# Performance work log

Measured on AMD Instinct MI355X. Metric: run time of the kernel, lower is better.

## Reference

```python
import jax, jax.numpy as jnp
import numpy as np

N = 100000       # nodes
E = 3200000      # edges (before self-loops)
F_IN = 256       # input feature dim
HID = 32         # GCNConv output dim
CLASSES = 10


def setup_inputs() -> dict:
    key = jax.random.key(0)
    k1, k2, k3, k4 = jax.random.split(key, 4)
    feature = jax.random.normal(k1, (N, F_IN), dtype=jnp.float32)
    edge_index = jax.random.randint(k2, (2, E), 0, N, dtype=jnp.int64)
    W1 = jax.random.normal(k3, (F_IN, HID), dtype=jnp.float32) * (1.0 / np.sqrt(F_IN))
    b1 = jnp.zeros((HID,), dtype=jnp.float32)
    W2 = jax.random.normal(k4, (HID, CLASSES), dtype=jnp.float32) * (1.0 / np.sqrt(HID))
    b2 = jnp.zeros((CLASSES,), dtype=jnp.float32)
    return {"feature": feature, "edge_index": edge_index,
            "W1": W1, "b1": b1, "W2": W2, "b2": b2}


def reference(feature, edge_index, W1, b1, W2, b2):
    # --- GCNConv(features, 32): PyG semantics ---
    # add self-loops
    loops = jnp.arange(N, dtype=edge_index.dtype)
    row = jnp.concatenate([edge_index[0], loops])   # source nodes
    col = jnp.concatenate([edge_index[1], loops])   # target nodes
    # linear transform before propagation
    h = feature @ W1                                # [N, HID]
    # symmetric deg^{-1/2} normalization (degree counted at targets)
    deg = jax.ops.segment_sum(jnp.ones_like(col, dtype=h.dtype), col,
                              num_segments=N)       # [N], >=1 due to self-loops
    dinv = jax.lax.rsqrt(deg)
    norm = dinv[row] * dinv[col]                    # [E+N]
    # gather-scale-scatter aggregation
    msg = h[row] * norm[:, None]                    # [E+N, HID]
    agg = jax.ops.segment_sum(msg, col, num_segments=N) + b1  # [N, HID]
    # --- relu, (dropout: identity in eval), final linear, log_softmax ---
    act = jax.nn.relu(agg)
    logits = act @ W2 + b2                          # [N, CLASSES]
    return jax.nn.log_softmax(logits, axis=1)
```

## Files before the change

kernel.cpp:

```cpp
#include <hip/hip_runtime.h>
#include <hip/hip_fp16.h>

constexpr int N_NODES = 100000;
constexpr int E_EDGES = 3200000;
constexpr int F_IN    = 256;
constexpr int HID     = 32;
constexpr int NCLS    = 10;

constexpr int BUCK_SHIFT = 7;
constexpr int NPB        = 128;
constexpr int NBUCK      = (N_NODES + NPB - 1) / NPB;
constexpr int EPB        = 8192;
constexpr int NBLK1      = (E_EDGES + EPB - 1) / EPB;
constexpr int CAP        = 6144;

constexpr size_t OFF_FLAG = 0;
constexpr size_t OFF_GCUR = 4u << 10;
constexpr size_t OFF_W1F  = 32u << 10;
constexpr size_t OFF_CNT  = 1u << 20;
constexpr size_t OFF_OFF  = 3u << 20;
constexpr size_t OFF_DINV = 4u << 20;
constexpr size_t OFF_CSR  = 5u << 20;
constexpr size_t OFF_BIN  = 25u << 20;
constexpr size_t OFF_HS   = 25u << 20;

typedef __attribute__((ext_vector_type(8))) short bf16x8;
typedef __attribute__((ext_vector_type(4))) float f32x4;

__device__ __forceinline__ unsigned pack_bf16x2(float a, float b) {
    unsigned ua = __float_as_uint(a), ub = __float_as_uint(b);
    ua = (ua + 0x7FFFu + ((ua >> 16) & 1u)) >> 16;
    ub = (ub + 0x7FFFu + ((ub >> 16) & 1u)) >> 16;
    return ua | (ub << 16);
}
__device__ __forceinline__ __half2 u2h(unsigned u) {
    union { unsigned u; __half2 h; } v; v.u = u; return v.h;
}

__device__ __forceinline__ int load_idx(const void* ei, long long i, int is64) {
    if (is64) return (int)((const long long*)ei)[i];
    return ((const int*)ei)[i];
}

__global__ __launch_bounds__(1024) void k_initw(const int* __restrict__ ei32,
                                                int* __restrict__ flag,
                                                int* __restrict__ gcur,
                                                const float* __restrict__ W1,
                                                unsigned* __restrict__ w1f) {
    __shared__ int nz;
    int tid = threadIdx.x;
    if (tid == 0) nz = 0;
    __syncthreads();
    if (ei32[2 * tid + 1] != 0) atomicOr(&nz, 1);
    __syncthreads();
    if (tid == 0) flag[0] = (nz == 0) ? 1 : 0;
    if (tid < NBUCK) gcur[tid] = tid * CAP;

    #pragma unroll
    for (int q = 0; q < 4; q++) {
        int i = tid + q * 1024;
        int p    = i & 3;
        int lane = (i >> 2) & 63;
        int f    = i >> 8;
        int ks = f >> 1, t = f & 1;
        int kg = lane >> 4, col = lane & 15;
        int k0 = ks * 32 + kg * 8 + p * 2;
        float w0 = W1[k0 * HID + t * 16 + col];
        float w1 = W1[(k0 + 1) * HID + t * 16 + col];
        w1f[i] = pack_bf16x2(w0, w1);
    }
}

__global__ __launch_bounds__(1024) void k_scat(const void* __restrict__ ei,
                                               const int* __restrict__ flag,
                                               int* __restrict__ gcur,
                                               unsigned* __restrict__ binned) {
    __shared__ int h[NBUCK];
    __shared__ int cur[NBUCK];
    int tid = threadIdx.x, blk = blockIdx.x;
    for (int i = tid; i < NBUCK; i += 1024) h[i] = 0;
    __syncthreads();

    int is64 = flag[0];
    int base = blk * EPB;
    int nedge = min(EPB, E_EDGES - base);

    unsigned val[8];
    int      bk[8];
    #pragma unroll
    for (int j = 0; j < 8; j++) {
        int k = tid + j * 1024;
        if (k < nedge) {
            int i = base + k;
            int r = load_idx(ei, i, is64);
            int c = load_idx(ei, (long long)E_EDGES + i, is64);
            bk[j]  = c >> BUCK_SHIFT;
            val[j] = ((unsigned)r << BUCK_SHIFT) | ((unsigned)c & (NPB - 1));
            atomicAdd(&h[bk[j]], 1);
        } else {
            bk[j] = -1;
        }
    }
    __syncthreads();

    for (int j = tid; j < NBUCK; j += 1024) {
        int c = h[j];
        cur[j] = (c > 0) ? atomicAdd(&gcur[j], c) : 0;
    }
    __syncthreads();

    #pragma unroll
    for (int j = 0; j < 8; j++) {
        if (bk[j] >= 0) {
            int d = atomicAdd(&cur[bk[j]], 1);
            binned[d] = val[j];
        }
    }
}

__global__ __launch_bounds__(1024) void k_p2(const unsigned* __restrict__ binned,
                                             const int* __restrict__ gcur,
                                             int* __restrict__ cnt,
                                             int* __restrict__ off,
                                             float* __restrict__ dinv,
                                             int* __restrict__ csr) {
    __shared__ unsigned sval[CAP];
    __shared__ int lcnt[NPB], sc[NPB], lcur[NPB];
    int b = blockIdx.x, tid = threadIdx.x;
    int s = b * CAP;
    int m = gcur[b] - s;
    if (tid < NPB) lcnt[tid] = 0;
    __syncthreads();
    for (int i = tid; i < m; i += 1024) {
        unsigned p = binned[s + i];
        sval[i] = p;
        atomicAdd(&lcnt[p & (NPB - 1)], 1);
    }
    __syncthreads();
    if (tid < NPB) sc[tid] = lcnt[tid];
    __syncthreads();
    for (int d = 1; d < NPB; d <<= 1) {
        int t = 0;
        if (tid < NPB && tid >= d) t = sc[tid - d];
        __syncthreads();
        if (tid < NPB) sc[tid] += t;
        __syncthreads();
    }
    if (tid < NPB) {
        int o = s + sc[tid] - lcnt[tid];
        lcur[tid] = o;
        int node = b * NPB + tid;
        if (node < N_NODES) {
            off[node]  = o;
            cnt[node]  = lcnt[tid];
            dinv[node] = rsqrtf((float)lcnt[tid] + 1.0f);
        }
    }
    __syncthreads();
    for (int i = tid; i < m; i += 1024) {
        unsigned p = sval[i];
        int pos = atomicAdd(&lcur[p & (NPB - 1)], 1);
        csr[pos] = (int)(p >> BUCK_SHIFT);
    }
}

__global__ __launch_bounds__(256) void k_h(const float* __restrict__ feat,
                                           const unsigned* __restrict__ w1f,
                                           const float* __restrict__ dinv,
                                           unsigned short* __restrict__ hs16s) {
    int tid  = threadIdx.x;
    int lane = tid & 63;
    long wid = (long)blockIdx.x * 4 + (tid >> 6);
    int n0 = (int)(wid * 16);
    if (n0 >= N_NODES) return;

    bf16x8 bfrag[16];
    const bf16x8* wv = (const bf16x8*)w1f;
    #pragma unroll
    for (int f = 0; f < 16; f++) bfrag[f] = wv[f * 64 + lane];

    int arow = lane & 15;
    int kg   = lane >> 4;
    const float4* fr = (const float4*)(feat + (size_t)(n0 + arow) * F_IN);

    f32x4 acc0 = {0.f, 0.f, 0.f, 0.f};
    f32x4 acc1 = {0.f, 0.f, 0.f, 0.f};

    #pragma unroll
    for (int ks = 0; ks < 8; ks++) {
        float4 fa = fr[ks * 8 + kg * 2 + 0];
        float4 fb = fr[ks * 8 + kg * 2 + 1];
        unsigned au[4];
        au[0] = pack_bf16x2(fa.x, fa.y);
        au[1] = pack_bf16x2(fa.z, fa.w);
        au[2] = pack_bf16x2(fb.x, fb.y);
        au[3] = pack_bf16x2(fb.z, fb.w);
        bf16x8 af = *(bf16x8*)au;
        acc0 = __builtin_amdgcn_mfma_f32_16x16x32_bf16(af, bfrag[ks * 2 + 0], acc0, 0, 0, 0);
        acc1 = __builtin_amdgcn_mfma_f32_16x16x32_bf16(af, bfrag[ks * 2 + 1], acc1, 0, 0, 0);
    }

    int rb = kg * 4;
    #pragma unroll
    for (int r = 0; r < 4; r++) {
        int node = n0 + rb + r;
        float di = dinv[node];
        hs16s[(size_t)node * HID + arow]      = __half_as_ushort(__float2half(acc0[r] * di));
        hs16s[(size_t)node * HID + 16 + arow] = __half_as_ushort(__float2half(acc1[r] * di));
    }
}

__global__ __launch_bounds__(256) void k_aggout(const int* __restrict__ off,
                                                const int* __restrict__ cnt,
                                                const int* __restrict__ csr,
                                                const unsigned* __restrict__ hs16,
                                                const float* __restrict__ dinv,
                                                const float* __restrict__ b1,
                                                const float* __restrict__ W2,
                                                const float* __restrict__ b2,
                                                float* __restrict__ out) {
    __shared__ float W2s[HID * NCLS];
    __shared__ float b2s[NCLS];
    int tid = threadIdx.x;
    for (int i = tid; i < HID * NCLS; i += 256) W2s[i] = W2[i];
    if (tid < NCLS) b2s[tid] = b2[tid];
    __syncthreads();

    int l2   = tid & 3;
    int g    = tid >> 2;
    int node = blockIdx.x * 64 + g;
    if (node >= N_NODES) return;

    int o = off[node];
    int n = cnt[node];

    const uint4* hsv = (const uint4*)hs16;
    uint4 ps = hsv[(size_t)node * 4 + l2];
    __half2 s0 = u2h(ps.x), s1 = u2h(ps.y), s2 = u2h(ps.z), s3 = u2h(ps.w);

    #define ADDQ(Q) \
        s0 = __hadd2(s0, u2h(Q.x)); s1 = __hadd2(s1, u2h(Q.y)); \
        s2 = __hadd2(s2, u2h(Q.z)); s3 = __hadd2(s3, u2h(Q.w));

    int i = 0;
    for (; i + 8 <= n; i += 8) {
        int r0 = csr[o + i + 0];
        int r1 = csr[o + i + 1];
        int r2 = csr[o + i + 2];
        int r3 = csr[o + i + 3];
        int r4 = csr[o + i + 4];
        int r5 = csr[o + i + 5];
        int r6 = csr[o + i + 6];
        int r7 = csr[o + i + 7];
        uint4 q0 = hsv[(size_t)r0 * 4 + l2];
        uint4 q1 = hsv[(size_t)r1 * 4 + l2];
        uint4 q2 = hsv[(size_t)r2 * 4 + l2];
        uint4 q3 = hsv[(size_t)r3 * 4 + l2];
        uint4 q4 = hsv[(size_t)r4 * 4 + l2];
        uint4 q5 = hsv[(size_t)r5 * 4 + l2];
        uint4 q6 = hsv[(size_t)r6 * 4 + l2];
        uint4 q7 = hsv[(size_t)r7 * 4 + l2];
        ADDQ(q0) ADDQ(q1) ADDQ(q2) ADDQ(q3)
        ADDQ(q4) ADDQ(q5) ADDQ(q6) ADDQ(q7)
    }
    for (; i < n; i++) {
        uint4 q = hsv[(size_t)csr[o + i] * 4 + l2];
        ADDQ(q)
    }
    #undef ADDQ

    float2 f0 = __half22float2(s0);
    float2 f1 = __half22float2(s1);
    float2 f2 = __half22float2(s2);
    float2 f3 = __half22float2(s3);

    float di = dinv[node];
    float4 b1lo = *(const float4*)(b1 + 8 * l2);
    float4 b1hi = *(const float4*)(b1 + 8 * l2 + 4);
    float act[8];
    act[0] = fmaxf(b1lo.x + f0.x * di, 0.f);
    act[1] = fmaxf(b1lo.y + f0.y * di, 0.f);
    act[2] = fmaxf(b1lo.z + f1.x * di, 0.f);
    act[3] = fmaxf(b1lo.w + f1.y * di, 0.f);
    act[4] = fmaxf(b1hi.x + f2.x * di, 0.f);
    act[5] = fmaxf(b1hi.y + f2.y * di, 0.f);
    act[6] = fmaxf(b1hi.z + f3.x * di, 0.f);
    act[7] = fmaxf(b1hi.w + f3.y * di, 0.f);

    float p[NCLS];
    #pragma unroll
    for (int c = 0; c < NCLS; c++) {
        float s = 0.f;
        #pragma unroll
        for (int k = 0; k < 8; k++) s = fmaf(act[k], W2s[(8 * l2 + k) * NCLS + c], s);
        p[c] = s;
    }

    #pragma unroll
    for (int d = 1; d < 4; d <<= 1) {
        #pragma unroll
        for (int c = 0; c < NCLS; c++) p[c] += __shfl_xor(p[c], d, 4);
    }

    #pragma unroll
    for (int c = 0; c < NCLS; c++) p[c] += b2s[c];
    float m = p[0];
    #pragma unroll
    for (int c = 1; c < NCLS; c++) m = fmaxf(m, p[c]);
    float se = 0.f;
    #pragma unroll
    for (int c = 0; c < NCLS; c++) se += expf(p[c] - m);
    float lse = m + logf(se);

    #pragma unroll
    for (int q = 0; q < 3; q++) {
        int c = l2 + 4 * q;
        if (c < NCLS) {
            float v = p[0];
            #pragma unroll
            for (int cc = 1; cc < NCLS; cc++) v = (c == cc) ? p[cc] : v;
            out[(size_t)node * NCLS + c] = v - lse;
        }
    }
}

extern "C" void kernel_launch(void* const* d_in, const int* in_sizes, int n_in,
                              void* d_out, int out_size, void* d_ws, size_t ws_size,
                              hipStream_t stream) {
    const float* feat = (const float*)d_in[0];
    const void*  ei   = d_in[1];
    const float* W1   = (const float*)d_in[2];
    const float* b1   = (const float*)d_in[3];
    const float* W2   = (const float*)d_in[4];
    const float* b2   = (const float*)d_in[5];
    float* out = (float*)d_out;

    char* ws = (char*)d_ws;
    int*      flag   = (int*)(ws + OFF_FLAG);
    int*      gcur   = (int*)(ws + OFF_GCUR);
    unsigned* w1f    = (unsigned*)(ws + OFF_W1F);
    int*      cnt    = (int*)(ws + OFF_CNT);
    int*      off    = (int*)(ws + OFF_OFF);
    float*    dinv   = (float*)(ws + OFF_DINV);
    int*      csr    = (int*)(ws + OFF_CSR);
    unsigned* binned = (unsigned*)(ws + OFF_BIN);
    unsigned* hs16   = (unsigned*)(ws + OFF_HS);

    k_initw<<<1, 1024, 0, stream>>>((const int*)ei, flag, gcur, W1, w1f);
    k_scat<<<NBLK1, 1024, 0, stream>>>(ei, flag, gcur, binned);
    k_p2<<<NBUCK, 1024, 0, stream>>>(binned, gcur, cnt, off, dinv, csr);

    k_h<<<(N_NODES / 16 + 3) / 4, 256, 0, stream>>>(feat, w1f, dinv,
                                                    (unsigned short*)hs16);
    k_aggout<<<(N_NODES + 63) / 64, 256, 0, stream>>>(off, cnt, csr, hs16, dinv,
                                                      b1, W2, b2, out);
}
```

Before: 119.8 us.

## Split hidden features into two halves and aggregate in two cache-friendly passes

The fp16 hidden feature table is stored as two separate 16-column halves. Aggregation runs as two kernels, each gathering only one half, so each pass works on a smaller gather table that may fit better in L2 and cut the miss traffic of random neighbor gathers. The first pass writes partial logits to a workspace buffer, and the second adds them before log_softmax. The cost is reading the CSR index array and offsets twice, plus an extra partial-logit write and read. The feature transform kernel now handles 32 nodes per wave so it can write both halves.

```diff
diff --git a/kernel.cpp b/kernel.cpp
--- a/kernel.cpp
+++ b/kernel.cpp
@@ -22,7 +22,9 @@
 constexpr size_t OFF_DINV = 4u << 20;
 constexpr size_t OFF_CSR  = 5u << 20;
 constexpr size_t OFF_BIN  = 25u << 20;
-constexpr size_t OFF_HS   = 25u << 20;
+constexpr size_t OFF_HSA  = 25u << 20;
+constexpr size_t OFF_HSB  = 29u << 20;
+constexpr size_t OFF_PART = 33u << 20;
 
 typedef __attribute__((ext_vector_type(8))) short bf16x8;
 typedef __attribute__((ext_vector_type(4))) float f32x4;
@@ -167,11 +169,12 @@
 __global__ __launch_bounds__(256) void k_h(const float* __restrict__ feat,
                                            const unsigned* __restrict__ w1f,
                                            const float* __restrict__ dinv,
-                                           unsigned short* __restrict__ hs16s) {
+                                           unsigned short* __restrict__ hsA,
+                                           unsigned short* __restrict__ hsB) {
     int tid  = threadIdx.x;
     int lane = tid & 63;
     long wid = (long)blockIdx.x * 4 + (tid >> 6);
-    int n0 = (int)(wid * 16);
+    int n0 = (int)(wid * 32);
     if (n0 >= N_NODES) return;
 
     bf16x8 bfrag[16];
@@ -181,44 +184,142 @@
 
     int arow = lane & 15;
     int kg   = lane >> 4;
-    const float4* fr = (const float4*)(feat + (size_t)(n0 + arow) * F_IN);
-
-    f32x4 acc0 = {0.f, 0.f, 0.f, 0.f};
-    f32x4 acc1 = {0.f, 0.f, 0.f, 0.f};
+    const float4* frA = (const float4*)(feat + (size_t)(n0 + arow) * F_IN);
+    const float4* frB = (const float4*)(feat + (size_t)(n0 + 16 + arow) * F_IN);
+
+    f32x4 acc0a = {0.f, 0.f, 0.f, 0.f};
+    f32x4 acc1a = {0.f, 0.f, 0.f, 0.f};
+    f32x4 acc0b = {0.f, 0.f, 0.f, 0.f};
+    f32x4 acc1b = {0.f, 0.f, 0.f, 0.f};
 
     #pragma unroll
     for (int ks = 0; ks < 8; ks++) {
-        float4 fa = fr[ks * 8 + kg * 2 + 0];
-        float4 fb = fr[ks * 8 + kg * 2 + 1];
-        unsigned au[4];
-        au[0] = pack_bf16x2(fa.x, fa.y);
-        au[1] = pack_bf16x2(fa.z, fa.w);
-        au[2] = pack_bf16x2(fb.x, fb.y);
-        au[3] = pack_bf16x2(fb.z, fb.w);
-        bf16x8 af = *(bf16x8*)au;
-        acc0 = __builtin_amdgcn_mfma_f32_16x16x32_bf16(af, bfrag[ks * 2 + 0], acc0, 0, 0, 0);
-        acc1 = __builtin_amdgcn_mfma_f32_16x16x32_bf16(af, bfrag[ks * 2 + 1], acc1, 0, 0, 0);
+        float4 faA = frA[ks * 8 + kg * 2 + 0];
+        float4 fbA = frA[ks * 8 + kg * 2 + 1];
+        float4 faB = frB[ks * 8 + kg * 2 + 0];
+        float4 fbB = frB[ks * 8 + kg * 2 + 1];
+        unsigned auA[4], auB[4];
+        auA[0] = pack_bf16x2(faA.x, faA.y);
+        auA[1] = pack_bf16x2(faA.z, faA.w);
+        auA[2] = pack_bf16x2(fbA.x, fbA.y);
+        auA[3] = pack_bf16x2(fbA.z, fbA.w);
+        auB[0] = pack_bf16x2(faB.x, faB.y);
+        auB[1] = pack_bf16x2(faB.z, faB.w);
+        auB[2] = pack_bf16x2(fbB.x, fbB.y);
+        auB[3] = pack_bf16x2(fbB.z, fbB.w);
+        bf16x8 afA = *(bf16x8*)auA;
+        bf16x8 afB = *(bf16x8*)auB;
+        acc0a = __builtin_amdgcn_mfma_f32_16x16x32_bf16(afA, bfrag[ks * 2 + 0], acc0a, 0, 0, 0);
+        acc1a = __builtin_amdgcn_mfma_f32_16x16x32_bf16(afA, bfrag[ks * 2 + 1], acc1a, 0, 0, 0);
+        acc0b = __builtin_amdgcn_mfma_f32_16x16x32_bf16(afB, bfrag[ks * 2 + 0], acc0b, 0, 0, 0);
+        acc1b = __builtin_amdgcn_mfma_f32_16x16x32_bf16(afB, bfrag[ks * 2 + 1], acc1b, 0, 0, 0);
     }
 
     int rb = kg * 4;
     #pragma unroll
     for (int r = 0; r < 4; r++) {
-        int node = n0 + rb + r;
-        float di = dinv[node];
-        hs16s[(size_t)node * HID + arow]      = __half_as_ushort(__float2half(acc0[r] * di));
-        hs16s[(size_t)node * HID + 16 + arow] = __half_as_ushort(__float2half(acc1[r] * di));
-    }
-}
-
-__global__ __launch_bounds__(256) void k_aggout(const int* __restrict__ off,
-                                                const int* __restrict__ cnt,
-                                                const int* __restrict__ csr,
-                                                const unsigned* __restrict__ hs16,
-                                                const float* __restrict__ dinv,
-                                                const float* __restrict__ b1,
-                                                const float* __restrict__ W2,
-                                                const float* __restrict__ b2,
-                                                float* __restrict__ out) {
+        int nodeA = n0 + rb + r;
+        float diA = dinv[nodeA];
+        hsA[(size_t)nodeA * 16 + arow] = __half_as_ushort(__float2half(acc0a[r] * diA));
+        hsB[(size_t)nodeA * 16 + arow] = __half_as_ushort(__float2half(acc1a[r] * diA));
+        int nodeB = n0 + 16 + rb + r;
+        float diB = dinv[nodeB];
+        hsA[(size_t)nodeB * 16 + arow] = __half_as_ushort(__float2half(acc0b[r] * diB));
+        hsB[(size_t)nodeB * 16 + arow] = __half_as_ushort(__float2half(acc1b[r] * diB));
+    }
+}
+
+__global__ __launch_bounds__(256) void k_aggA(const int* __restrict__ off,
+                                              const int* __restrict__ cnt,
+                                              const int* __restrict__ csr,
+                                              const unsigned short* __restrict__ hsA,
+                                              const float* __restrict__ dinv,
+                                              const float* __restrict__ b1,
+                                              const float* __restrict__ W2,
+                                              float* __restrict__ partial) {
+    __shared__ float W2s[HID * NCLS];
+    int tid = threadIdx.x;
+    for (int i = tid; i < HID * NCLS; i += 256) W2s[i] = W2[i];
+    __syncthreads();
+
+    int l    = tid & 1;
+    int g    = tid >> 1;
+    int node = blockIdx.x * 128 + g;
+    if (node >= N_NODES) return;
+
+    int o = off[node];
+    int n = cnt[node];
+
+    const uint4* hv = (const uint4*)hsA;
+    uint4 ps = hv[(size_t)node * 2 + l];
+    __half2 s0 = u2h(ps.x), s1 = u2h(ps.y), s2 = u2h(ps.z), s3 = u2h(ps.w);
+
+    #define ADDQ(Q) \
+        s0 = __hadd2(s0, u2h(Q.x)); s1 = __hadd2(s1, u2h(Q.y)); \
+        s2 = __hadd2(s2, u2h(Q.z)); s3 = __hadd2(s3, u2h(Q.w));
+    int i = 0;
+    for (; i + 8 <= n; i += 8) {
+        int r0 = csr[o + i + 0], r1 = csr[o + i + 1], r2 = csr[o + i + 2], r3 = csr[o + i + 3];
+        int r4 = csr[o + i + 4], r5 = csr[o + i + 5], r6 = csr[o + i + 6], r7 = csr[o + i + 7];
+        uint4 q0 = hv[(size_t)r0 * 2 + l], q1 = hv[(size_t)r1 * 2 + l];
+        uint4 q2 = hv[(size_t)r2 * 2 + l], q3 = hv[(size_t)r3 * 2 + l];
+        uint4 q4 = hv[(size_t)r4 * 2 + l], q5 = hv[(size_t)r5 * 2 + l];
+        uint4 q6 = hv[(size_t)r6 * 2 + l], q7 = hv[(size_t)r7 * 2 + l];
+        ADDQ(q0) ADDQ(q1) ADDQ(q2) ADDQ(q3) ADDQ(q4) ADDQ(q5) ADDQ(q6) ADDQ(q7)
+    }
+    for (; i < n; i++) {
+        uint4 q = hv[(size_t)csr[o + i] * 2 + l];
+        ADDQ(q)
+    }
+    #undef ADDQ
+
+    float2 f0 = __half22float2(s0), f1 = __half22float2(s1);
+    float2 f2 = __half22float2(s2), f3 = __half22float2(s3);
+    float di = dinv[node];
+    int kb = 8 * l;
+    float4 blo = *(const float4*)(b1 + kb);
+    float4 bhi = *(const float4*)(b1 + kb + 4);
+    float act[8];
+    act[0] = fmaxf(blo.x + f0.x * di, 0.f);
+    act[1] = fmaxf(blo.y + f0.y * di, 0.f);
+    act[2] = fmaxf(blo.z + f1.x * di, 0.f);
+    act[3] = fmaxf(blo.w + f1.y * di, 0.f);
+    act[4] = fmaxf(bhi.x + f2.x * di, 0.f);
+    act[5] = fmaxf(bhi.y + f2.y * di, 0.f);
+    act[6] = fmaxf(bhi.z + f3.x * di, 0.f);
+    act[7] = fmaxf(bhi.w + f3.y * di, 0.f);
+
+    float p[NCLS];
+    #pragma unroll
+    for (int c = 0; c < NCLS; c++) {
+        float s = 0.f;
+        #pragma unroll
+        for (int k = 0; k < 8; k++) s = fmaf(act[k], W2s[(kb + k) * NCLS + c], s);
+        p[c] = s;
+    }
+    #pragma unroll
+    for (int c = 0; c < NCLS; c++) p[c] += __shfl_xor(p[c], 1, 2);
+
+    #pragma unroll
+    for (int j = 0; j < 5; j++) {
+        int c = 5 * l + j;
+        float v = p[0];
+        #pragma unroll
+        for (int cc = 1; cc < NCLS; cc++) v = (c == cc) ? p[cc] : v;
+        partial[(size_t)node * NCLS + c] = v;
+    }
+}
+
+__global__ __launch_bounds__(256) void k_aggB(const int* __restrict__ off,
+                                              const int* __restrict__ cnt,
+                                              const int* __restrict__ csr,
+                                              const unsigned short* __restrict__ hsB,
+                                              const float* __restrict__ dinv,
+                                              const float* __restrict__ b1,
+                                              const float* __restrict__ W2,
+                                              const float* __restrict__ b2,
+                                              const float* __restrict__ partial,
+                                              float* __restrict__ out) {
     __shared__ float W2s[HID * NCLS];
     __shared__ float b2s[NCLS];
     int tid = threadIdx.x;
@@ -226,84 +327,68 @@
     if (tid < NCLS) b2s[tid] = b2[tid];
     __syncthreads();
 
-    int l2   = tid & 3;
-    int g    = tid >> 2;
-    int node = blockIdx.x * 64 + g;
+    int l    = tid & 1;
+    int g    = tid >> 1;
+    int node = blockIdx.x * 128 + g;
     if (node >= N_NODES) return;
 
     int o = off[node];
     int n = cnt[node];
 
-    const uint4* hsv = (const uint4*)hs16;
-    uint4 ps = hsv[(size_t)node * 4 + l2];
+    const uint4* hv = (const uint4*)hsB;
+    uint4 ps = hv[(size_t)node * 2 + l];
     __half2 s0 = u2h(ps.x), s1 = u2h(ps.y), s2 = u2h(ps.z), s3 = u2h(ps.w);
 
     #define ADDQ(Q) \
         s0 = __hadd2(s0, u2h(Q.x)); s1 = __hadd2(s1, u2h(Q.y)); \
         s2 = __hadd2(s2, u2h(Q.z)); s3 = __hadd2(s3, u2h(Q.w));
-
     int i = 0;
     for (; i + 8 <= n; i += 8) {
-        int r0 = csr[o + i + 0];
-        int r1 = csr[o + i + 1];
-        int r2 = csr[o + i + 2];
-        int r3 = csr[o + i + 3];
-        int r4 = csr[o + i + 4];
-        int r5 = csr[o + i + 5];
-        int r6 = csr[o + i + 6];
-        int r7 = csr[o + i + 7];
-        uint4 q0 = hsv[(size_t)r0 * 4 + l2];
-        uint4 q1 = hsv[(size_t)r1 * 4 + l2];
-        uint4 q2 = hsv[(size_t)r2 * 4 + l2];
-        uint4 q3 = hsv[(size_t)r3 * 4 + l2];
-        uint4 q4 = hsv[(size_t)r4 * 4 + l2];
-        uint4 q5 = hsv[(size_t)r5 * 4 + l2];
-        uint4 q6 = hsv[(size_t)r6 * 4 + l2];
-        uint4 q7 = hsv[(size_t)r7 * 4 + l2];
-        ADDQ(q0) ADDQ(q1) ADDQ(q2) ADDQ(q3)
-        ADDQ(q4) ADDQ(q5) ADDQ(q6) ADDQ(q7)
+        int r0 = csr[o + i + 0], r1 = csr[o + i + 1], r2 = csr[o + i + 2], r3 = csr[o + i + 3];
+        int r4 = csr[o + i + 4], r5 = csr[o + i + 5], r6 = csr[o + i + 6], r7 = csr[o + i + 7];
+        uint4 q0 = hv[(size_t)r0 * 2 + l], q1 = hv[(size_t)r1 * 2 + l];
+        uint4 q2 = hv[(size_t)r2 * 2 + l], q3 = hv[(size_t)r3 * 2 + l];
+        uint4 q4 = hv[(size_t)r4 * 2 + l], q5 = hv[(size_t)r5 * 2 + l];
+        uint4 q6 = hv[(size_t)r6 * 2 + l], q7 = hv[(size_t)r7 * 2 + l];
+        ADDQ(q0) ADDQ(q1) ADDQ(q2) ADDQ(q3) ADDQ(q4) ADDQ(q5) ADDQ(q6) ADDQ(q7)
     }
     for (; i < n; i++) {
-        uint4 q = hsv[(size_t)csr[o + i] * 4 + l2];
+        uint4 q = hv[(size_t)csr[o + i] * 2 + l];
         ADDQ(q)
     }
     #undef ADDQ
 
-    float2 f0 = __half22float2(s0);
-    float2 f1 = __half22float2(s1);
-    float2 f2 = __half22float2(s2);
-    float2 f3 = __half22float2(s3);
-
+    float2 f0 = __half22float2(s0), f1 = __half22float2(s1);
+    float2 f2 = __half22float2(s2), f3 = __half22float2(s3);
     float di = dinv[node];
-    float4 b1lo = *(const float4*)(b1 + 8 * l2);
-    float4 b1hi = *(const float4*)(b1 + 8 * l2 + 4);
+    int kb = 16 + 8 * l;
+    float4 blo = *(const float4*)(b1 + kb);
+    float4 bhi = *(const float4*)(b1 + kb + 4);
     float act[8];
-    act[0] = fmaxf(b1lo.x + f0.x * di, 0.f);
-    act[1] = fmaxf(b1lo.y + f0.y * di, 0.f);
-    act[2] = fmaxf(b1lo.z + f1.x * di, 0.f);
-    act[3] = fmaxf(b1lo.w + f1.y * di, 0.f);
-    act[4] = fmaxf(b1hi.x + f2.x * di, 0.f);
-    act[5] = fmaxf(b1hi.y + f2.y * di, 0.f);
-    act[6] = fmaxf(b1hi.z + f3.x * di, 0.f);
-    act[7] = fmaxf(b1hi.w + f3.y * di, 0.f);
+    act[0] = fmaxf(blo.x + f0.x * di, 0.f);
+    act[1] = fmaxf(blo.y + f0.y * di, 0.f);
+    act[2] = fmaxf(blo.z + f1.x * di, 0.f);
+    act[3] = fmaxf(blo.w + f1.y * di, 0.f);
+    act[4] = fmaxf(bhi.x + f2.x * di, 0.f);
+    act[5] = fmaxf(bhi.y + f2.y * di, 0.f);
+    act[6] = fmaxf(bhi.z + f3.x * di, 0.f);
+    act[7] = fmaxf(bhi.w + f3.y * di, 0.f);
 
     float p[NCLS];
     #pragma unroll
     for (int c = 0; c < NCLS; c++) {
         float s = 0.f;
         #pragma unroll
-        for (int k = 0; k < 8; k++) s = fmaf(act[k], W2s[(8 * l2 + k) * NCLS + c], s);
+        for (int k = 0; k < 8; k++) s = fmaf(act[k], W2s[(kb + k) * NCLS + c], s);
         p[c] = s;
     }
-
-    #pragma unroll
-    for (int d = 1; d < 4; d <<= 1) {
-        #pragma unroll
-        for (int c = 0; c < NCLS; c++) p[c] += __shfl_xor(p[c], d, 4);
-    }
-
-    #pragma unroll
-    for (int c = 0; c < NCLS; c++) p[c] += b2s[c];
+    #pragma unroll
+    for (int c = 0; c < NCLS; c++) p[c] += __shfl_xor(p[c], 1, 2);
+
+    #pragma unroll
+    for (int c = 0; c < NCLS; c++)
+        p[c] += partial[(size_t)node * NCLS + c] + b2s[c];
+
     float m = p[0];
     #pragma unroll
     for (int c = 1; c < NCLS; c++) m = fmaxf(m, p[c]);
@@ -313,14 +398,12 @@
     float lse = m + logf(se);
 
     #pragma unroll
-    for (int q = 0; q < 3; q++) {
-        int c = l2 + 4 * q;
-        if (c < NCLS) {
-            float v = p[0];
-            #pragma unroll
-            for (int cc = 1; cc < NCLS; cc++) v = (c == cc) ? p[cc] : v;
-            out[(size_t)node * NCLS + c] = v - lse;
-        }
+    for (int j = 0; j < 5; j++) {
+        int c = 5 * l + j;
+        float v = p[0];
+        #pragma unroll
+        for (int cc = 1; cc < NCLS; cc++) v = (c == cc) ? p[cc] : v;
+        out[(size_t)node * NCLS + c] = v - lse;
     }
 }
 
@@ -336,22 +419,25 @@
     float* out = (float*)d_out;
 
     char* ws = (char*)d_ws;
-    int*      flag   = (int*)(ws + OFF_FLAG);
-    int*      gcur   = (int*)(ws + OFF_GCUR);
-    unsigned* w1f    = (unsigned*)(ws + OFF_W1F);
-    int*      cnt    = (int*)(ws + OFF_CNT);
-    int*      off    = (int*)(ws + OFF_OFF);
-    float*    dinv   = (float*)(ws + OFF_DINV);
-    int*      csr    = (int*)(ws + OFF_CSR);
-    unsigned* binned = (unsigned*)(ws + OFF_BIN);
-    unsigned* hs16   = (unsigned*)(ws + OFF_HS);
+    int*            flag    = (int*)(ws + OFF_FLAG);
+    int*            gcur    = (int*)(ws + OFF_GCUR);
+    unsigned*       w1f     = (unsigned*)(ws + OFF_W1F);
+    int*            cnt     = (int*)(ws + OFF_CNT);
+    int*            off     = (int*)(ws + OFF_OFF);
+    float*          dinv    = (float*)(ws + OFF_DINV);
+    int*            csr     = (int*)(ws + OFF_CSR);
+    unsigned*       binned  = (unsigned*)(ws + OFF_BIN);
+    unsigned short* hsA     = (unsigned short*)(ws + OFF_HSA);
+    unsigned short* hsB     = (unsigned short*)(ws + OFF_HSB);
+    float*          partial = (float*)(ws + OFF_PART);
 
     k_initw<<<1, 1024, 0, stream>>>((const int*)ei, flag, gcur, W1, w1f);
     k_scat<<<NBLK1, 1024, 0, stream>>>(ei, flag, gcur, binned);
     k_p2<<<NBUCK, 1024, 0, stream>>>(binned, gcur, cnt, off, dinv, csr);
 
-    k_h<<<(N_NODES / 16 + 3) / 4, 256, 0, stream>>>(feat, w1f, dinv,
-                                                    (unsigned short*)hs16);
-    k_aggout<<<(N_NODES + 63) / 64, 256, 0, stream>>>(off, cnt, csr, hs16, dinv,
-                                                      b1, W2, b2, out);
-}
+    k_h<<<(N_NODES / 32 + 3) / 4, 256, 0, stream>>>(feat, w1f, dinv, hsA, hsB);
+    k_aggA<<<(N_NODES + 127) / 128, 256, 0, stream>>>(off, cnt, csr, hsA, dinv,
+                                                      b1, W2, partial);
+    k_aggB<<<(N_NODES + 127) / 128, 256, 0, stream>>>(off, cnt, csr, hsB, dinv,
+                                                      b1, W2, b2, partial, out);
+}
```

Result: slower. 144.5 us (+20.6%).
